# Performance work log

Hardware: AMD Instinct MI355X
Metric: run time of the kernel (lower is better)

Reference implementation:

```python
import jax, jax.numpy as jnp
import numpy as np

MGC_SIZE = 80
COND_DIM = 256
LSTM_SIZE = 500
UP_SCALE = 64  # prod([4,4,4])
TEMPERATURE = 1.0
EPS_MIN = -7.0


def setup_inputs() -> dict:
    key = jax.random.key(0)
    ks = jax.random.split(key, 10)
    B, T_FRAMES = 16, 32
    T = T_FRAMES * UP_SCALE  # 2048 decode steps
    s = 0.02  # weight scale for numerical stability (logvar goes through exp)
    return {
        "mgc": jax.random.normal(ks[0], (B, T_FRAMES, MGC_SIZE), dtype=jnp.float32),
        "eps": jax.random.normal(ks[1], (B, T), dtype=jnp.float32),
        # UpsampleNet stand-in: linear projection mgc_size->256, then repeat x64 in time
        "W_up": jax.random.normal(ks[2], (MGC_SIZE, COND_DIM), dtype=jnp.float32) * s,
        "b_up": jnp.zeros((COND_DIM,), dtype=jnp.float32),
        # LSTM (PyTorch layout, gate order i,f,g,o)
        "W_ih": jax.random.normal(ks[3], (4 * LSTM_SIZE, COND_DIM + 1), dtype=jnp.float32) * s,
        "W_hh": jax.random.normal(ks[4], (4 * LSTM_SIZE, LSTM_SIZE), dtype=jnp.float32) * s,
        "b_ih": jax.random.normal(ks[5], (4 * LSTM_SIZE,), dtype=jnp.float32) * s,
        "b_hh": jax.random.normal(ks[6], (4 * LSTM_SIZE,), dtype=jnp.float32) * s,
        # output Linear(lstm_size, 2)
        "W_out": jax.random.normal(ks[7], (2, LSTM_SIZE), dtype=jnp.float32) * s,
        "b_out": jnp.zeros((2,), dtype=jnp.float32),
    }


def reference(mgc, eps, W_up, b_up, W_ih, W_hh, b_ih, b_hh, W_out, b_out):
    B = mgc.shape[0]
    # conditioning: (B, T_frames, 80) -> (B, T, 256)
    cond = jnp.repeat(mgc @ W_up + b_up, UP_SCALE, axis=1)
    bias = b_ih + b_hh

    def step(carry, xs):
        h, c, x_prev = carry              # (B,H), (B,H), (B,)
        cond_t, eps_t = xs                # (B,256), (B,)
        inp = jnp.concatenate([cond_t, x_prev[:, None]], axis=1)  # (B,257)
        gates = inp @ W_ih.T + h @ W_hh.T + bias                  # (B,4H)
        i, f, g, o = jnp.split(gates, 4, axis=1)
        i = jax.nn.sigmoid(i)
        f = jax.nn.sigmoid(f)
        g = jnp.tanh(g)
        o = jax.nn.sigmoid(o)
        c = f * c + i * g
        h = o * jnp.tanh(c)
        out = h @ W_out.T + b_out         # (B,2)
        mean = jnp.tanh(out[:, 0])
        logvar = jnp.maximum(out[:, 1], EPS_MIN)  # clamp(min=eps_min)
        zz = mean + (eps_t * TEMPERATURE) * jnp.exp(logvar)
        return (h, c, zz), (mean, logvar, zz)

    h0 = jnp.zeros((B, LSTM_SIZE), dtype=mgc.dtype)
    c0 = jnp.zeros((B, LSTM_SIZE), dtype=mgc.dtype)
    x0 = jnp.zeros((B,), dtype=mgc.dtype)
    xs = (cond.transpose(1, 0, 2), eps.T)  # time-major
    _, (mean, logvar, zz) = jax.lax.scan(step, (h0, c0, x0), xs)
    # back to (B, T)
    return mean.T, logvar.T, zz.T
```

## Files before the change

kernel.cpp:

```cpp
#include <hip/hip_runtime.h>
#include <stdint.h>

#define TSTEPS 2048
#define NB     16
#define HDIM   500
#define NSLICE 16
#define NTHR   256
#define NBLK   256
#define GSTR   20
#define HSTR   264

#define HBASE(P) ((size_t)(P) * 4096)
#define DONE64   8192
#define ELECT64  8193

typedef __attribute__((ext_vector_type(8))) short s16x8;
typedef __attribute__((ext_vector_type(4))) float f32x4;
typedef __attribute__((ext_vector_type(4))) unsigned int u32x4;

__device__ __forceinline__ unsigned short f2bf(float f) {
    unsigned u = __float_as_uint(f);
    u += 0x7FFFu + ((u >> 16) & 1u);
    return (unsigned short)(u >> 16);
}
__device__ __forceinline__ float sigm(float x)   { return __fdividef(1.f, 1.f + __expf(-x)); }
__device__ __forceinline__ float tanhf_(float x) { return 1.f - __fdividef(2.f, __expf(2.f * x) + 1.f); }

__global__ void zero_ws_kernel(uint32_t* p, int n) {
    int i = blockIdx.x * blockDim.x + threadIdx.x;
    if (i < n) p[i] = 0u;
}

__global__ __launch_bounds__(NTHR, 1) void wavernn_persist(
    const float* __restrict__ mgc,  const float* __restrict__ eps,
    const float* __restrict__ Wup,  const float* __restrict__ bup,
    const float* __restrict__ Wih,  const float* __restrict__ Whh,
    const float* __restrict__ bih,  const float* __restrict__ bhh,
    const float* __restrict__ Wout, const float* __restrict__ bout,
    float* __restrict__ out, uint64_t* __restrict__ hb)
{
    if (blockIdx.x >= NSLICE) {
        const uint64_t* done = hb + DONE64;
        float a = (float)threadIdx.x * 1e-3f + (float)blockIdx.x;
        for (int it = 0; it < 100000; ++it) {
            if (__hip_atomic_load(done, __ATOMIC_RELAXED,
                                  __HIP_MEMORY_SCOPE_AGENT) != 0ull) break;
            #pragma unroll 16
            for (int i = 0; i < 4096; ++i) a = __builtin_fmaf(a, 1.0000001f, 1e-7f);
        }
        asm volatile("" :: "v"(a));
        return;
    }

    const int s    = blockIdx.x;
    const int tid  = threadIdx.x;
    const int lane = tid & 63;
    const int wave = tid >> 6;
    const int l16  = lane & 15;
    const int g    = lane >> 4;

    __shared__ __align__(16) uint32_t h_l[16 * HSTR];
    __shared__ __align__(16) float gates_l[NB * 132];
    __shared__ __align__(16) float gcond[128 * GSTR];
    __shared__ __align__(16) float condT[256 * NB];
    __shared__ __align__(16) float mgcl[NB * 80];
    __shared__ __align__(16) float eps_l[128 * NB];
    __shared__ __align__(16) float zz_l[NB];
    __shared__ __align__(16) uint32_t part0_l[16 * 17];
    __shared__ __align__(16) uint32_t part1_l[16 * 17];
    __shared__ __align__(16) float stage_m[1024];
    __shared__ __align__(16) float stage_v[1024];
    __shared__ __align__(16) float stage_z[1024];

    s16x8 bfr[2][16];
    float wihl[2];
    #pragma unroll
    for (int t2 = 0; t2 < 2; ++t2) {
        const int q    = t2 * 16 + l16;
        const int hidx = s * 32 + q;
        const bool valid = hidx < HDIM;
        const int grow = wave * HDIM + hidx;
        wihl[t2] = valid ? Wih[grow * 257 + 256] : 0.f;
        #pragma unroll
        for (int kk = 0; kk < 16; ++kk) {
            const int k0 = kk * 32 + g * 8;
            s16x8 r;
            #pragma unroll
            for (int j = 0; j < 8; ++j) {
                const int k = k0 + j;
                const float v = (valid && k < HDIM) ? Whh[grow * HDIM + k] : 0.f;
                r[j] = (short)f2bf(v);
            }
            bfr[t2][kk] = r;
        }
    }
    const int b_e = tid >> 4;
    const int qh  = tid & 15;
    const int q0  = 2 * qh, q1 = q0 + 1;
    const int k0g = s * 32 + q0, k1g = s * 32 + q1;
    const float w0q0 = (k0g < HDIM) ? Wout[k0g]        : 0.f;
    const float w0q1 = (k1g < HDIM) ? Wout[k1g]        : 0.f;
    const float w1q0 = (k0g < HDIM) ? Wout[HDIM + k0g] : 0.f;
    const float w1q1 = (k1g < HDIM) ? Wout[HDIM + k1g] : 0.f;
    const float bout0 = bout[0], bout1 = bout[1];
    float cst0 = 0.f, cst1 = 0.f;

    auto rebuild = [&](int f) {
        for (int i = tid; i < NB * 80; i += NTHR) {
            const int b = i / 80, m = i - b * 80;
            mgcl[i] = mgc[(b * 32 + f) * 80 + m];
        }
        for (int i = tid; i < 64 * NB; i += NTHR) {
            const int st = i >> 4, b = i & 15;
            eps_l[((f & 1) * 64 + st) * NB + b] = eps[b * 2048 + f * 64 + st];
        }
        __syncthreads();
        {
            const int c = tid;
            float a[NB];
            #pragma unroll
            for (int b = 0; b < NB; ++b) a[b] = bup[c];
            for (int m = 0; m < 80; ++m) {
                const float w = Wup[m * 256 + c];
                #pragma unroll
                for (int b = 0; b < NB; ++b) a[b] += mgcl[b * 80 + m] * w;
            }
            #pragma unroll
            for (int b = 0; b < NB; ++b) condT[c * NB + b] = a[b];
        }
        __syncthreads();
        {
            const int n = tid >> 1, kc = tid & 1;
            const int gate = n >> 5, q = n & 31;
            const int hidx = s * 32 + q;
            const bool valid = hidx < HDIM;
            const int grow = gate * HDIM + hidx;
            float a[NB];
            #pragma unroll
            for (int b = 0; b < NB; ++b) a[b] = 0.f;
            if (valid) {
                const float* wr = Wih + (size_t)grow * 257 + kc * 128;
                for (int k = 0; k < 128; ++k) {
                    const float w = wr[k];
                    const float* cp = &condT[(kc * 128 + k) * NB];
                    #pragma unroll
                    for (int b = 0; b < NB; ++b) a[b] += cp[b] * w;
                }
            }
            if (kc == 0) {
                const float bias = valid ? (bih[grow] + bhh[grow]) : 0.f;
                #pragma unroll
                for (int b = 0; b < NB; ++b) gcond[n * GSTR + b] = a[b] + bias;
            }
            __syncthreads();
            if (kc == 1) {
                #pragma unroll
                for (int b = 0; b < NB; ++b) gcond[n * GSTR + b] += a[b];
            }
        }
        __syncthreads();
    };

    for (int i = tid; i < 16 * HSTR; i += NTHR) h_l[i] = 0u;
    rebuild(0);

    const int gp = tid >> 4, gb = tid & 15;

    for (int t = 0; t <= TSTEPS; ++t) {
        if (t == TSTEPS && s != 0) break;

        if (t > 0) {
            const uint32_t* src = (const uint32_t*)(hb + HBASE((t & 1) ^ 1)
                                                    + (size_t)(gp * 16 + gb) * 16);
            const uint32_t want12 = (uint32_t)t & 0xFFFu;
            u32x4 u[8];
            int guard = 0;
            while (true) {
                #pragma unroll
                for (int i = 0; i < 8; ++i)
                    asm volatile("global_load_dwordx4 %0, %1, off sc0 sc1"
                                 : "=v"(u[i]) : "v"(src + i * 4));
                asm volatile("s_waitcnt vmcnt(0)" ::: "memory");
                __builtin_amdgcn_sched_barrier(0);
                bool ok = true;
                #pragma unroll
                for (int i = 0; i < 8; ++i)
                    ok &= ((u[i][1] & 0xFFFu) == want12) & ((u[i][3] & 0xFFFu) == want12);
                if (ok || ++guard > (1 << 14)) break;
                if (guard > 4) __builtin_amdgcn_s_sleep(1);
            }
            #pragma unroll
            for (int c = 0; c < 4; ++c) {
                u32x4 w;
                w[0] = u[2 * c][0];     w[1] = u[2 * c][2];
                w[2] = u[2 * c + 1][0]; w[3] = u[2 * c + 1][2];
                *(u32x4*)&h_l[gp * HSTR + (c * 16 + gb) * 4] = w;
            }
            part0_l[gp * 17 + gb] = ((u[0][1] >> 12) & 0xFFFFu)
                                  | (((u[0][3] >> 12) & 0xFFFFu) << 16);
            part1_l[gp * 17 + gb] = ((u[1][1] >> 12) & 0xFFFFu)
                                  | (((u[1][3] >> 12) & 0xFFFFu) << 16);
        }
        __syncthreads();

        if (t > 0) {
            float o0[4], o1[4];
            #pragma unroll
            for (int j = 0; j < 4; ++j) {
                o0[j] = __uint_as_float(part0_l[l16 * 17 + (g * 4 + j)]);
                o1[j] = __uint_as_float(part1_l[l16 * 17 + (g * 4 + j)]);
            }
            #pragma unroll
            for (int m = 1; m < 16; m <<= 1) {
                #pragma unroll
                for (int j = 0; j < 4; ++j) {
                    o0[j] += __shfl_xor(o0[j], m);
                    o1[j] += __shfl_xor(o1[j], m);
                }
            }
            const int row = (t - 1) & 127;
            const int r64 = (t - 1) & 63;
            #pragma unroll
            for (int j = 0; j < 4; ++j) {
                const int B = g * 4 + j;
                const float mean = tanhf_(o0[j] + bout0);
                const float lv   = fmaxf(o1[j] + bout1, -7.f);
                const float zzv  = mean + eps_l[row * NB + B] * __expf(lv);
                if (l16 == 0) {
                    zz_l[B] = zzv;
                    if (s == 0) {
                        stage_m[r64 * 16 + B] = mean;
                        stage_v[r64 * 16 + B] = lv;
                        stage_z[r64 * 16 + B] = zzv;
                    }
                }
            }
            __builtin_amdgcn_sched_barrier(0);
        }

        if (t == TSTEPS) {
            __syncthreads();
            for (int k = tid; k < 1024; k += NTHR) {
                const int r = k >> 4, b = k & 15;
                out[         b * 2048 + 31 * 64 + r] = stage_m[k];
                out[32768 +  b * 2048 + 31 * 64 + r] = stage_v[k];
                out[65536 +  b * 2048 + 31 * 64 + r] = stage_z[k];
            }
            if (tid == 0)
                __hip_atomic_store(hb + DONE64, 1ull,
                                   __ATOMIC_RELAXED, __HIP_MEMORY_SCOPE_AGENT);
            break;
        }

        const int n0 = wave * 32 + l16;
        f32x4 acc0a = *(const f32x4*)&gcond[n0 * GSTR + g * 4];
        f32x4 acc1a = *(const f32x4*)&gcond[(n0 + 16) * GSTR + g * 4];
        f32x4 acc0b = {0.f, 0.f, 0.f, 0.f};
        f32x4 acc1b = {0.f, 0.f, 0.f, 0.f};
        s16x8 hfr[16];
        #pragma unroll
        for (int p = 0; p < 16; ++p)
            hfr[p] = *(const s16x8*)&h_l[p * HSTR + lane * 4];
        #pragma unroll
        for (int kk = 0; kk < 8; ++kk) {
            acc0a = __builtin_amdgcn_mfma_f32_16x16x32_bf16(hfr[kk],     bfr[0][kk],     acc0a, 0, 0, 0);
            acc1a = __builtin_amdgcn_mfma_f32_16x16x32_bf16(hfr[kk],     bfr[1][kk],     acc1a, 0, 0, 0);
            acc0b = __builtin_amdgcn_mfma_f32_16x16x32_bf16(hfr[kk + 8], bfr[0][kk + 8], acc0b, 0, 0, 0);
            acc1b = __builtin_amdgcn_mfma_f32_16x16x32_bf16(hfr[kk + 8], bfr[1][kk + 8], acc1b, 0, 0, 0);
        }
        f32x4 r0 = acc0a + acc0b;
        f32x4 r1 = acc1a + acc1b;
        if (t > 0) {
            const f32x4 zzq = *(const f32x4*)&zz_l[g * 4];
            r0 += zzq * wihl[0];
            r1 += zzq * wihl[1];
        }
        #pragma unroll
        for (int v = 0; v < 4; ++v) {
            gates_l[(g * 4 + v) * 132 + n0]      = r0[v];
            gates_l[(g * 4 + v) * 132 + n0 + 16] = r1[v];
        }
        __syncthreads();

        {
            const uint32_t tag12 = (uint32_t)(t + 1) & 0xFFFu;
            float po0, po1;
            uint32_t hp = 0;
            {
                const float gi = gates_l[b_e * 132 +      q0];
                const float gf = gates_l[b_e * 132 + 32 + q0];
                const float gg = gates_l[b_e * 132 + 64 + q0];
                const float go = gates_l[b_e * 132 + 96 + q0];
                cst0 = sigm(gf) * cst0 + sigm(gi) * tanhf_(gg);
                const float h = sigm(go) * tanhf_(cst0);
                if (k0g < HDIM) hp |= (uint32_t)f2bf(h);
                po0 = h * w0q0; po1 = h * w1q0;
            }
            {
                const float gi = gates_l[b_e * 132 +      q1];
                const float gf = gates_l[b_e * 132 + 32 + q1];
                const float gg = gates_l[b_e * 132 + 64 + q1];
                const float go = gates_l[b_e * 132 + 96 + q1];
                cst1 = sigm(gf) * cst1 + sigm(gi) * tanhf_(gg);
                const float h = sigm(go) * tanhf_(cst1);
                if (k1g < HDIM) hp |= ((uint32_t)f2bf(h)) << 16;
                po0 += h * w0q1; po1 += h * w1q1;
            }
            po0 += __shfl_xor(po0, 1);  po1 += __shfl_xor(po1, 1);
            po0 += __shfl_xor(po0, 2);  po1 += __shfl_xor(po1, 2);
            po0 += __shfl_xor(po0, 4);  po1 += __shfl_xor(po1, 4);
            po0 += __shfl_xor(po0, 8);  po1 += __shfl_xor(po1, 8);
            uint32_t piece = 0;
            if (qh < 4) {
                const uint32_t pb = (qh < 2) ? __float_as_uint(po0) : __float_as_uint(po1);
                piece = (pb >> ((qh & 1) * 16)) & 0xFFFFu;
            }
            const uint64_t rec = (uint64_t)hp | ((uint64_t)tag12 << 32)
                               | ((uint64_t)piece << 44);
            __hip_atomic_store(hb + HBASE(t & 1) + ((size_t)(s * 16 + b_e) * 16 + qh),
                               rec, __ATOMIC_RELAXED, __HIP_MEMORY_SCOPE_AGENT);
        }

        if (s == 0 && t > 0 && (t & 63) == 0) {
            const int fo = (t >> 6) - 1;
            for (int k = tid; k < 1024; k += NTHR) {
                const int r = k >> 4, b = k & 15;
                out[         b * 2048 + fo * 64 + r] = stage_m[k];
                out[32768 +  b * 2048 + fo * 64 + r] = stage_v[k];
                out[65536 +  b * 2048 + fo * 64 + r] = stage_z[k];
            }
        }
        if (((t + 1) & 63) == 0 && (t + 1) < TSTEPS) rebuild((t + 1) >> 6);
    }
}

extern "C" void kernel_launch(void* const* d_in, const int* in_sizes, int n_in,
                              void* d_out, int out_size, void* d_ws, size_t ws_size,
                              hipStream_t stream) {
    const float* mgc  = (const float*)d_in[0];
    const float* eps  = (const float*)d_in[1];
    const float* Wup  = (const float*)d_in[2];
    const float* bup  = (const float*)d_in[3];
    const float* Wih  = (const float*)d_in[4];
    const float* Whh  = (const float*)d_in[5];
    const float* bih  = (const float*)d_in[6];
    const float* bhh  = (const float*)d_in[7];
    const float* Wout = (const float*)d_in[8];
    const float* bout = (const float*)d_in[9];

    uint64_t* hb = (uint64_t*)d_ws;

    zero_ws_kernel<<<65, 256, 0, stream>>>((uint32_t*)hb, 16388);
    wavernn_persist<<<NBLK, NTHR, 0, stream>>>(mgc, eps, Wup, bup, Wih, Whh,
                                               bih, bhh, Wout, bout,
                                               (float*)d_out, hb);
}
```

Before: 9.166 ms.

## Read own slice's hidden state from LDS and sleep most idle filler blocks

Each working block now keeps its own published h records in shared memory and reads its own slice from there, so it no longer polls global memory for data it produced itself. This costs an extra __syncthreads per step. Filler blocks 64 and above now idle with s_sleep instead of spinning FMAs, which reduces power and contention while blocks 16-63 still keep clocks up. The workspace zeroing count shrinks because the unused ELECT slot was removed.

```diff
diff --git a/kernel.cpp b/kernel.cpp
--- a/kernel.cpp
+++ b/kernel.cpp
@@ -12,7 +12,6 @@
 
 #define HBASE(P) ((size_t)(P) * 4096)
 #define DONE64   8192
-#define ELECT64  8193
 
 typedef __attribute__((ext_vector_type(8))) short s16x8;
 typedef __attribute__((ext_vector_type(4))) float f32x4;
@@ -41,14 +40,23 @@
 {
     if (blockIdx.x >= NSLICE) {
         const uint64_t* done = hb + DONE64;
-        float a = (float)threadIdx.x * 1e-3f + (float)blockIdx.x;
-        for (int it = 0; it < 100000; ++it) {
-            if (__hip_atomic_load(done, __ATOMIC_RELAXED,
-                                  __HIP_MEMORY_SCOPE_AGENT) != 0ull) break;
-            #pragma unroll 16
-            for (int i = 0; i < 4096; ++i) a = __builtin_fmaf(a, 1.0000001f, 1e-7f);
-        }
-        asm volatile("" :: "v"(a));
+        if (blockIdx.x < 64) {
+            float a = (float)threadIdx.x * 1e-3f + (float)blockIdx.x;
+            for (int it = 0; it < 100000; ++it) {
+                if (__hip_atomic_load(done, __ATOMIC_RELAXED,
+                                      __HIP_MEMORY_SCOPE_AGENT) != 0ull) break;
+                #pragma unroll 16
+                for (int i = 0; i < 4096; ++i) a = __builtin_fmaf(a, 1.0000001f, 1e-7f);
+            }
+            asm volatile("" :: "v"(a));
+        } else {
+            for (int it = 0; it < 50000; ++it) {
+                if (__hip_atomic_load(done, __ATOMIC_RELAXED,
+                                      __HIP_MEMORY_SCOPE_AGENT) != 0ull) break;
+                #pragma unroll
+                for (int ss = 0; ss < 8; ++ss) __builtin_amdgcn_s_sleep(127);
+            }
+        }
         return;
     }
 
@@ -66,6 +74,7 @@
     __shared__ __align__(16) float mgcl[NB * 80];
     __shared__ __align__(16) float eps_l[128 * NB];
     __shared__ __align__(16) float zz_l[NB];
+    __shared__ __align__(16) uint64_t pub_l[256];
     __shared__ __align__(16) uint32_t part0_l[16 * 17];
     __shared__ __align__(16) uint32_t part1_l[16 * 17];
     __shared__ __align__(16) float stage_m[1024];
@@ -170,36 +179,57 @@
         if (t == TSTEPS && s != 0) break;
 
         if (t > 0) {
-            const uint32_t* src = (const uint32_t*)(hb + HBASE((t & 1) ^ 1)
-                                                    + (size_t)(gp * 16 + gb) * 16);
-            const uint32_t want12 = (uint32_t)t & 0xFFFu;
-            u32x4 u[8];
-            int guard = 0;
-            while (true) {
-                #pragma unroll
-                for (int i = 0; i < 8; ++i)
-                    asm volatile("global_load_dwordx4 %0, %1, off sc0 sc1"
-                                 : "=v"(u[i]) : "v"(src + i * 4));
-                asm volatile("s_waitcnt vmcnt(0)" ::: "memory");
-                __builtin_amdgcn_sched_barrier(0);
-                bool ok = true;
-                #pragma unroll
-                for (int i = 0; i < 8; ++i)
-                    ok &= ((u[i][1] & 0xFFFu) == want12) & ((u[i][3] & 0xFFFu) == want12);
-                if (ok || ++guard > (1 << 14)) break;
-                if (guard > 4) __builtin_amdgcn_s_sleep(1);
-            }
-            #pragma unroll
-            for (int c = 0; c < 4; ++c) {
-                u32x4 w;
-                w[0] = u[2 * c][0];     w[1] = u[2 * c][2];
-                w[2] = u[2 * c + 1][0]; w[3] = u[2 * c + 1][2];
-                *(u32x4*)&h_l[gp * HSTR + (c * 16 + gb) * 4] = w;
-            }
-            part0_l[gp * 17 + gb] = ((u[0][1] >> 12) & 0xFFFFu)
-                                  | (((u[0][3] >> 12) & 0xFFFFu) << 16);
-            part1_l[gp * 17 + gb] = ((u[1][1] >> 12) & 0xFFFFu)
-                                  | (((u[1][3] >> 12) & 0xFFFFu) << 16);
+            if (gp == s) {
+                const uint64_t r0 = pub_l[gb * 16 + 0], r1 = pub_l[gb * 16 + 1];
+                const uint64_t r2 = pub_l[gb * 16 + 2], r3 = pub_l[gb * 16 + 3];
+                uint32_t lo[16];
+                lo[0] = (uint32_t)r0; lo[1] = (uint32_t)r1;
+                lo[2] = (uint32_t)r2; lo[3] = (uint32_t)r3;
+                #pragma unroll
+                for (int j = 4; j < 16; ++j) lo[j] = (uint32_t)pub_l[gb * 16 + j];
+                #pragma unroll
+                for (int c = 0; c < 4; ++c) {
+                    u32x4 w;
+                    w[0] = lo[4 * c]; w[1] = lo[4 * c + 1];
+                    w[2] = lo[4 * c + 2]; w[3] = lo[4 * c + 3];
+                    *(u32x4*)&h_l[gp * HSTR + (c * 16 + gb) * 4] = w;
+                }
+                part0_l[gp * 17 + gb] = (((uint32_t)(r0 >> 32) >> 12) & 0xFFFFu)
+                                      | ((((uint32_t)(r1 >> 32) >> 12) & 0xFFFFu) << 16);
+                part1_l[gp * 17 + gb] = (((uint32_t)(r2 >> 32) >> 12) & 0xFFFFu)
+                                      | ((((uint32_t)(r3 >> 32) >> 12) & 0xFFFFu) << 16);
+            } else {
+                const uint32_t* src = (const uint32_t*)(hb + HBASE((t & 1) ^ 1)
+                                                        + (size_t)(gp * 16 + gb) * 16);
+                const uint32_t want12 = (uint32_t)t & 0xFFFu;
+                u32x4 u[8];
+                int guard = 0;
+                while (true) {
+                    #pragma unroll
+                    for (int i = 0; i < 8; ++i)
+                        asm volatile("global_load_dwordx4 %0, %1, off sc0 sc1"
+                                     : "=v"(u[i]) : "v"(src + i * 4));
+                    asm volatile("s_waitcnt vmcnt(0)" ::: "memory");
+                    __builtin_amdgcn_sched_barrier(0);
+                    bool ok = true;
+                    #pragma unroll
+                    for (int i = 0; i < 8; ++i)
+                        ok &= ((u[i][1] & 0xFFFu) == want12) & ((u[i][3] & 0xFFFu) == want12);
+                    if (ok || ++guard > (1 << 14)) break;
+                    if (guard > 4) __builtin_amdgcn_s_sleep(1);
+                }
+                #pragma unroll
+                for (int c = 0; c < 4; ++c) {
+                    u32x4 w;
+                    w[0] = u[2 * c][0];     w[1] = u[2 * c][2];
+                    w[2] = u[2 * c + 1][0]; w[3] = u[2 * c + 1][2];
+                    *(u32x4*)&h_l[gp * HSTR + (c * 16 + gb) * 4] = w;
+                }
+                part0_l[gp * 17 + gb] = ((u[0][1] >> 12) & 0xFFFFu)
+                                      | (((u[0][3] >> 12) & 0xFFFFu) << 16);
+                part1_l[gp * 17 + gb] = ((u[1][1] >> 12) & 0xFFFFu)
+                                      | (((u[1][3] >> 12) & 0xFFFFu) << 16);
+            }
         }
         __syncthreads();
 
@@ -319,7 +349,9 @@
                                | ((uint64_t)piece << 44);
             __hip_atomic_store(hb + HBASE(t & 1) + ((size_t)(s * 16 + b_e) * 16 + qh),
                                rec, __ATOMIC_RELAXED, __HIP_MEMORY_SCOPE_AGENT);
-        }
+            pub_l[b_e * 16 + qh] = rec;
+        }
+        __syncthreads();
 
         if (s == 0 && t > 0 && (t & 63) == 0) {
             const int fo = (t >> 6) - 1;
@@ -350,7 +382,7 @@
 
     uint64_t* hb = (uint64_t*)d_ws;
 
-    zero_ws_kernel<<<65, 256, 0, stream>>>((uint32_t*)hb, 16388);
+    zero_ws_kernel<<<65, 256, 0, stream>>>((uint32_t*)hb, 16386);
     wavernn_persist<<<NBLK, NTHR, 0, stream>>>(mgc, eps, Wup, bup, Wih, Whh,
                                                bih, bhh, Wout, bout,
                                                (float*)d_out, hb);
```

New measurement: 9.024 ms. About the same (-1.6%).
